# Kernel optimization log

Measured on AMD Instinct MI355X. Metric: run time of the kernel, lower is better.

## Reference

```python
import jax, jax.numpy as jnp
import numpy as np

N_HEADS = 32
N_KV = 8
HEAD_DIM = 128
EPS = 1e-5

def _rope(t, fr, fi):
    # t: [b,s,h,hd] -> pairs [b,s,h,hd/2,2]; fr/fi: [s,hd/2]
    tp = t.astype(jnp.float32).reshape(*t.shape[:-1], HEAD_DIM // 2, 2)
    a, b = tp[..., 0], tp[..., 1]
    fr = fr[None, :, None, :]
    fi = fi[None, :, None, :]
    out = jnp.stack([a * fr - b * fi, a * fi + b * fr], axis=-1)
    return out.reshape(t.shape).astype(t.dtype)

def _rmsnorm(t):
    tf = t.astype(jnp.float32)
    return (tf * jax.lax.rsqrt(jnp.mean(tf * tf, axis=-1, keepdims=True) + EPS)).astype(t.dtype)

def setup_inputs() -> dict:
    key = jax.random.key(0)
    ks = jax.random.split(key, 5)
    b, s, dim = 1, 2048, 4096
    x = jax.random.normal(ks[0], (b, s, dim), dtype=jnp.float32) * 0.02
    wq = jax.random.normal(ks[1], (dim, dim), dtype=jnp.float32) * 0.02
    wk = jax.random.normal(ks[2], (N_KV * HEAD_DIM, dim), dtype=jnp.float32) * 0.02
    wv = jax.random.normal(ks[3], (N_KV * HEAD_DIM, dim), dtype=jnp.float32) * 0.02
    wo = jax.random.normal(ks[4], (dim, dim), dtype=jnp.float32) * 0.02
    # RoPE freqs, llama-style theta=10000
    inv = 1.0 / (10000.0 ** (np.arange(0, HEAD_DIM, 2, dtype=np.float32) / HEAD_DIM))
    ang = np.outer(np.arange(s, dtype=np.float32), inv)  # [s, hd/2]
    freqs_cis = jnp.asarray(np.stack([np.cos(ang), np.sin(ang)], axis=-1))  # [s, hd/2, 2]
    # causal additive mask
    mask = jnp.where(jnp.tril(jnp.ones((s, s), dtype=bool)), 0.0, -1e30).astype(jnp.float32)
    return {"x": x, "wq": wq, "wk": wk, "wv": wv, "wo": wo,
            "freqs_cis": freqs_cis, "mask": mask, "start_pos": 0}

def reference(x, wq, wk, wv, wo, freqs_cis, mask, start_pos):
    b, s, dim = x.shape
    n_rep = N_HEADS // N_KV
    xq = jnp.einsum('bsd,ed->bse', x, wq).reshape(b, s, N_HEADS, HEAD_DIM)
    xk = jnp.einsum('bsd,ed->bse', x, wk).reshape(b, s, N_KV, HEAD_DIM)
    xv = jnp.einsum('bsd,ed->bse', x, wv).reshape(b, s, N_KV, HEAD_DIM)
    fr, fi = freqs_cis[..., 0], freqs_cis[..., 1]
    xq = _rope(xq, fr, fi)
    xk = _rope(xk, fr, fi)
    xq = _rmsnorm(xq)
    xk = _rmsnorm(xk)
    # start_pos=0 prefill: KV cache write/read is identity on xk/xv
    q = xq.transpose(0, 2, 1, 3).reshape(b, N_KV, n_rep, s, HEAD_DIM)  # grouped query heads
    k = xk.transpose(0, 2, 1, 3)  # [b, n_kv, s, hd]
    v = xv.transpose(0, 2, 1, 3)
    scores = jnp.einsum('bkrsd,bktd->bkrst', q, k) / np.sqrt(HEAD_DIM)
    scores = scores + mask[None, None, None, :, :]
    probs = jax.nn.softmax(scores, axis=-1)
    o = jnp.einsum('bkrst,bktd->bkrsd', probs, v)
    o = o.reshape(b, N_HEADS, s, HEAD_DIM).transpose(0, 2, 1, 3).reshape(b, s, dim)
    return jnp.einsum('bse,de->bsd', o, wo)
```

## Files before the change

### kernel.cpp

```cpp
#include <hip/hip_runtime.h>
#include <hip/hip_bf16.h>
#include <cstdint>
#include <cstddef>

using u16 = unsigned short;
using u32 = unsigned int;

typedef __attribute__((ext_vector_type(8))) __bf16 bf16x8;
typedef __attribute__((ext_vector_type(4))) float f32x4;
typedef __attribute__((ext_vector_type(2))) float f32x2;
typedef __attribute__((ext_vector_type(4))) u32 u32x4;

typedef const __attribute__((address_space(1))) void* gas_ptr;
typedef __attribute__((address_space(3))) void* las_ptr;

__device__ __forceinline__ void async_cp16(const void* g, void* l) {
  __builtin_amdgcn_global_load_lds((gas_ptr)g, (las_ptr)l, 16, 0, 0);
}

__device__ __forceinline__ float bf2f(u16 u) {
  u32 v = ((u32)u) << 16;
  return __builtin_bit_cast(float, v);
}
__device__ __forceinline__ u16 f2bf(float f) {
  u32 v = __builtin_bit_cast(u32, f);
  u32 r = (v + 0x7fffu + ((v >> 16) & 1u)) >> 16;
  return (u16)r;
}

__device__ __forceinline__ f32x4 mfma16(bf16x8 a, bf16x8 b, f32x4 c) {
  return __builtin_amdgcn_mfma_f32_16x16x32_bf16(a, b, c, 0, 0, 0);
}

__global__ __launch_bounds__(256) void cvt_f32_bf16(const float* __restrict__ in,
                                                    u16* __restrict__ out, int n8) {
  int i = blockIdx.x * blockDim.x + threadIdx.x;
  int stride = gridDim.x * blockDim.x;
  for (; i < n8; i += stride) {
    const float4* p = (const float4*)(in + (size_t)i * 8);
    float4 a = p[0], b = p[1];
    union { u16 us[8]; u32x4 v; } o;
    o.us[0] = f2bf(a.x); o.us[1] = f2bf(a.y); o.us[2] = f2bf(a.z); o.us[3] = f2bf(a.w);
    o.us[4] = f2bf(b.x); o.us[5] = f2bf(b.y); o.us[6] = f2bf(b.z); o.us[7] = f2bf(b.w);
    *(u32x4*)(out + (size_t)i * 8) = o.v;
  }
}

__global__ __launch_bounds__(256) void cvt4(const float* __restrict__ x,
                                            const float* __restrict__ wq,
                                            const float* __restrict__ wk,
                                            const float* __restrict__ wv,
                                            u16* __restrict__ xb,
                                            u16* __restrict__ wqkv) {
  const int B0 = 1048576;
  const int B1 = B0 + 2097152;
  const int B2 = B1 + 524288;
  const int B3 = B2 + 524288;
  int i = blockIdx.x * blockDim.x + threadIdx.x;
  int stride = gridDim.x * blockDim.x;
  for (; i < B3; i += stride) {
    const float* src; u16* dst; int j;
    if (i < B0)      { src = x;  dst = xb;                           j = i; }
    else if (i < B1) { src = wq; dst = wqkv;                         j = i - B0; }
    else if (i < B2) { src = wk; dst = wqkv + (size_t)4096 * 4096;   j = i - B1; }
    else             { src = wv; dst = wqkv + (size_t)5120 * 4096;   j = i - B2; }
    const float4* p = (const float4*)(src + (size_t)j * 8);
    float4 a = p[0], b = p[1];
    union { u16 us[8]; u32x4 v; } o;
    o.us[0] = f2bf(a.x); o.us[1] = f2bf(a.y); o.us[2] = f2bf(a.z); o.us[3] = f2bf(a.w);
    o.us[4] = f2bf(b.x); o.us[5] = f2bf(b.y); o.us[6] = f2bf(b.z); o.us[7] = f2bf(b.w);
    *(u32x4*)(dst + (size_t)j * 8) = o.v;
  }
}

template <bool F32OUT>
__global__ __launch_bounds__(256, 3) void gemm_bt(const u16* __restrict__ A,
                                                  const u16* __restrict__ B,
                                                  void* __restrict__ Cv,
                                                  int M, int N, int K) {
  __shared__ __align__(16) u16 As[128 * 64];
  __shared__ __align__(16) u16 Bs[128 * 64];
  const int tid = threadIdx.x;
  const int wave = tid >> 6, lane = tid & 63;
  const int quad = lane >> 4, c16 = lane & 15;

  const int mb = M >> 7, nb = N >> 7;
  const int per_xcd_n = nb >> 3;
  const int xcd = blockIdx.x & 7, lid = blockIdx.x >> 3;
  const int m_t = lid % mb, n_local = lid / mb;
  const int m0 = m_t * 128, n0 = (xcd * per_xcd_n + n_local) * 128;

  const int wm = (wave & 1) * 64, wn = (wave >> 1) * 64;

  f32x4 acc[4][4] = {};

  const u16* Ab = A + (size_t)m0 * K;
  const u16* Bb = B + (size_t)n0 * K;

  for (int k0 = 0; k0 < K; k0 += 64) {
    __syncthreads();
#pragma unroll
    for (int i = 0; i < 4; ++i) {
      int idx = tid + 256 * i;
      int row = idx >> 3, sg = (idx & 7) ^ (row & 7);
      async_cp16(Ab + (size_t)row * K + k0 + sg * 8, As + (size_t)idx * 8);
    }
#pragma unroll
    for (int i = 0; i < 4; ++i) {
      int idx = tid + 256 * i;
      int row = idx >> 3, sg = (idx & 7) ^ (row & 7);
      async_cp16(Bb + (size_t)row * K + k0 + sg * 8, Bs + (size_t)idx * 8);
    }
    asm volatile("s_waitcnt vmcnt(0)" ::: "memory");
    __syncthreads();

    bf16x8 af[4][2], bfr[4][2];
#pragma unroll
    for (int mt = 0; mt < 4; ++mt) {
      int row = wm + mt * 16 + c16;
#pragma unroll
      for (int c = 0; c < 2; ++c)
        af[mt][c] = *(const bf16x8*)(As + row * 64 + (((c * 4 + quad) ^ (row & 7)) * 8));
    }
#pragma unroll
    for (int nt = 0; nt < 4; ++nt) {
      int row = wn + nt * 16 + c16;
#pragma unroll
      for (int c = 0; c < 2; ++c)
        bfr[nt][c] = *(const bf16x8*)(Bs + row * 64 + (((c * 4 + quad) ^ (row & 7)) * 8));
    }
#pragma unroll
    for (int c = 0; c < 2; ++c)
#pragma unroll
      for (int mt = 0; mt < 4; ++mt)
#pragma unroll
        for (int nt = 0; nt < 4; ++nt)
          acc[mt][nt] = mfma16(af[mt][c], bfr[nt][c], acc[mt][nt]);
  }

#pragma unroll
  for (int mt = 0; mt < 4; ++mt) {
#pragma unroll
    for (int nt = 0; nt < 4; ++nt) {
#pragma unroll
      for (int r = 0; r < 4; ++r) {
        int gm = m0 + wm + mt * 16 + quad * 4 + r;
        int gn = n0 + wn + nt * 16 + c16;
        float v = acc[mt][nt][r];
        if (F32OUT)
          ((float*)Cv)[(size_t)gm * N + gn] = v;
        else
          ((u16*)Cv)[(size_t)gm * N + gn] = f2bf(v);
      }
    }
  }
}

__global__ __launch_bounds__(256) void transpose_v(const u16* __restrict__ in,
                                                   u16* __restrict__ out) {
  __shared__ __align__(16) u16 t[64 * 72];
  const int bs = blockIdx.x * 64;
  const int be = blockIdx.y * 64;
  const int tid = threadIdx.x;
  {
    const int row = tid >> 3, cc = tid & 7;
#pragma unroll
    for (int pp = 0; pp < 2; ++pp) {
      int r = row + 32 * pp;
      u32x4 v = *(const u32x4*)(in + (size_t)(bs + r) * 6144 + 5120 + be + cc * 8);
      *(u32x4*)(&t[r * 72 + ((cc ^ ((r >> 3) & 7)) * 8)]) = v;
    }
  }
  __syncthreads();
  {
    const int c0 = tid >> 3, rc = tid & 7;
#pragma unroll
    for (int pp = 0; pp < 2; ++pp) {
      int c = c0 + 32 * pp;
      union { u16 us[8]; u32x4 v; } o;
#pragma unroll
      for (int j = 0; j < 8; ++j)
        o.us[j] = t[(rc * 8 + j) * 72 + ((((c >> 3) ^ rc) * 8) + (c & 7))];
      *(u32x4*)(out + (size_t)(be + c) * 2048 + bs + rc * 8) = o.v;
    }
  }
}

__global__ __launch_bounds__(256) void rope_rms(const u16* __restrict__ in, int stride,
                                                u16* __restrict__ out,
                                                const float* __restrict__ freqs,
                                                int n_heads) {
  int gw = blockIdx.x * 4 + (threadIdx.x >> 6);
  int lane = threadIdx.x & 63;
  int s = gw / n_heads, h = gw % n_heads;
  u32 ab = *(const u32*)(in + (size_t)s * stride + h * 128 + lane * 2);
  float a = bf2f((u16)(ab & 0xffff));
  float b = bf2f((u16)(ab >> 16));
  f32x2 ff = *(const f32x2*)(freqs + (size_t)s * 128 + lane * 2);
  float ra = a * ff.x - b * ff.y;
  float rb = a * ff.y + b * ff.x;
  float ss = ra * ra + rb * rb;
#pragma unroll
  for (int m = 32; m; m >>= 1) ss += __shfl_xor(ss, m, 64);
  float r = rsqrtf(ss * (1.0f / 128.0f) + 1e-5f);
  u32 pk = (u32)f2bf(ra * r) | ((u32)f2bf(rb * r) << 16);
  *(u32*)(out + ((size_t)h * 2048 + s) * 128 + lane * 2) = pk;
}

#define SEQ 2048
__global__ __launch_bounds__(512, 2) void attn(const u16* __restrict__ Q,
                                               const u16* __restrict__ Kh,
                                               const u16* __restrict__ VT,
                                               u16* __restrict__ O) {
  __shared__ __align__(16) u16 Ks[2][64 * 128];
  __shared__ __align__(16) u16 Vs[2][128 * 64];
  __shared__ __align__(16) u16 Ps[8][32 * 64];
  const int tid = threadIdx.x;
  const int wave = tid >> 6, lane = tid & 63;
  const int quad = lane >> 4, c16 = lane & 15;
  const int bid = blockIdx.x;
  const int hk = bid & 7;
  const int rest = bid >> 3;
  const int hq = rest & 3;
  const int p = rest >> 2;
  const int h = hk * 4 + hq;

  const int wl = wave & 3, grp = wave >> 2;
  const int qt = grp ? p : (15 - p);
  const int q0w = qt * 128 + wl * 32;
  const int kend = (15 - p) * 128 + 128;

  const float sc = 0.12751743f;
  const float B = 16.5f;
  const u16* Kb = Kh + (size_t)hk * SEQ * 128;
  const u16* Vb = VT + (size_t)hk * 128 * SEQ;

  auto stage = [&](int t0, int b) __attribute__((always_inline)) {
#pragma unroll
    for (int i = 0; i < 2; ++i) {
      int idx = tid + 512 * i;
      int row = idx >> 4, sg = (idx & 15) ^ (row & 7);
      async_cp16(Kb + (size_t)(t0 + row) * 128 + sg * 8, &Ks[b][(size_t)idx * 8]);
    }
#pragma unroll
    for (int i = 0; i < 2; ++i) {
      int idx = tid + 512 * i;
      int row = idx >> 3, sg = (idx & 7) ^ (row & 7);
      async_cp16(Vb + (size_t)row * SEQ + t0 + sg * 8, &Vs[b][(size_t)idx * 8]);
    }
  };

  bf16x8 qfr[2][4];
  const u16* qbase = Q + (size_t)h * SEQ * 128;
#pragma unroll
  for (int g = 0; g < 2; ++g)
#pragma unroll
    for (int c = 0; c < 4; ++c)
      qfr[g][c] =
          *(const bf16x8*)(qbase + (size_t)(q0w + g * 16 + c16) * 128 + c * 32 + quad * 8);

  f32x4 o_acc[2][8] = {};
  float lsum[2][4] = {};

  stage(0, 0);

#pragma unroll 1
  for (int t0 = 0; t0 < kend; t0 += 64) {
    const int cur = (t0 >> 6) & 1;
    asm volatile("s_waitcnt vmcnt(0)" ::: "memory");
    __syncthreads();
    if (t0 + 64 < kend) stage(t0 + 64, cur ^ 1);

    if (t0 < q0w + 32) {
      f32x4 sa[2][4] = {};
      __builtin_amdgcn_s_setprio(1);
#pragma unroll
      for (int ct = 0; ct < 4; ++ct) {
        int t = ct * 16 + c16;
        int tbase = t * 128;
        int tsw = t & 7;
#pragma unroll
        for (int c = 0; c < 4; ++c) {
          bf16x8 kf = *(const bf16x8*)(&Ks[cur][tbase + (((c * 4 + quad) ^ tsw) * 8)]);
          sa[0][ct] = mfma16(qfr[0][c], kf, sa[0][ct]);
          sa[1][ct] = mfma16(qfr[1][c], kf, sa[1][ct]);
        }
      }
      __builtin_amdgcn_s_setprio(0);

      const bool diag = (t0 + 64 > q0w);
      auto soft = [&](bool masked) __attribute__((always_inline)) {
#pragma unroll
        for (int g = 0; g < 2; ++g) {
#pragma unroll
          for (int r = 0; r < 4; ++r) {
            int row = g * 16 + quad * 4 + r;
            int row_q = q0w + row;
            int rbase = row * 64;
            int rsw = row & 7;
#pragma unroll
            for (int ct = 0; ct < 4; ++ct) {
              float s = sa[g][ct][r];
              float arg = fmaf(s, sc, -B);
              if (masked) {
                int t_idx = t0 + ct * 16 + c16;
                arg = (t_idx <= row_q) ? arg : -1.0e30f;
              }
              float pe = exp2f(arg);
              lsum[g][r] += pe;
              u32 pb = (__builtin_bit_cast(u32, pe) + 0x8000u) >> 16;
              Ps[wave][rbase + (((ct * 2 + (c16 >> 3)) ^ rsw) * 8) + (c16 & 7)] = (u16)pb;
            }
          }
        }
      };
      if (diag) soft(true); else soft(false);
      asm volatile("s_waitcnt lgkmcnt(0)" ::: "memory");

      __builtin_amdgcn_s_setprio(1);
#pragma unroll
      for (int tc = 0; tc < 2; ++tc) {
        bf16x8 pf[2];
#pragma unroll
        for (int g = 0; g < 2; ++g) {
          int prow = g * 16 + c16;
          pf[g] = *(const bf16x8*)(&Ps[wave][prow * 64 + (((tc * 4 + quad) ^ (prow & 7)) * 8)]);
        }
#pragma unroll
        for (int nt = 0; nt < 8; ++nt) {
          int dl = nt * 16 + c16;
          bf16x8 vf = *(const bf16x8*)(&Vs[cur][dl * 64 + (((tc * 4 + quad) ^ (dl & 7)) * 8)]);
          o_acc[0][nt] = mfma16(pf[0], vf, o_acc[0][nt]);
          o_acc[1][nt] = mfma16(pf[1], vf, o_acc[1][nt]);
        }
      }
      __builtin_amdgcn_s_setprio(0);
    }
  }

#pragma unroll
  for (int g = 0; g < 2; ++g) {
#pragma unroll
    for (int r = 0; r < 4; ++r) {
      float l = lsum[g][r];
#pragma unroll
      for (int m = 1; m < 16; m <<= 1) l += __shfl_xor(l, m, 64);
      float inv = 1.0f / l;
      int s_idx = q0w + g * 16 + quad * 4 + r;
      u16* ob = O + (size_t)s_idx * 4096 + (size_t)h * 128;
#pragma unroll
      for (int nt = 0; nt < 8; ++nt) ob[nt * 16 + c16] = f2bf(o_acc[g][nt][r] * inv);
    }
  }
}

extern "C" void kernel_launch(void* const* d_in, const int* in_sizes, int n_in,
                              void* d_out, int out_size, void* d_ws, size_t ws_size,
                              hipStream_t stream) {
  const float* x  = (const float*)d_in[0];
  const float* wq = (const float*)d_in[1];
  const float* wk = (const float*)d_in[2];
  const float* wv = (const float*)d_in[3];
  const float* wo = (const float*)d_in[4];
  const float* fr = (const float*)d_in[5];
  float* out = (float*)d_out;

  const size_t S = 2048, D = 4096, KV = 1024, NQKV = D + 2 * KV;
  u16* p = (u16*)d_ws;
  u16* xb     = p; p += S * D;
  u16* wqkv   = p; p += NQKV * D;
  u16* qkvraw = p; p += S * NQKV;
  u16* qh     = p; p += S * D;
  u16* khh    = p; p += S * KV;
  u16* vt     = p; p += KV * S;
  u16* wob = wqkv;
  u16* ob  = qkvraw;

  cvt4<<<dim3(2048), dim3(256), 0, stream>>>(x, wq, wk, wv, xb, wqkv);

  gemm_bt<false><<<dim3((S / 128) * (NQKV / 128)), dim3(256), 0, stream>>>(
      xb, wqkv, (void*)qkvraw, (int)S, (int)NQKV, (int)D);

  {
    int n8 = (int)(D * D / 8);
    cvt_f32_bf16<<<dim3(2048), dim3(256), 0, stream>>>(wo, wob, n8);
  }

  transpose_v<<<dim3(32, 16), dim3(256), 0, stream>>>(qkvraw, vt);
  rope_rms<<<dim3((int)(S * 32 / 4)), dim3(256), 0, stream>>>(qkvraw, (int)NQKV, qh, fr, 32);
  rope_rms<<<dim3((int)(S * 8 / 4)), dim3(256), 0, stream>>>(qkvraw + D, (int)NQKV, khh, fr, 8);

  attn<<<dim3(256), dim3(512), 0, stream>>>(qh, khh, vt, ob);

  gemm_bt<true><<<dim3((S / 128) * (D / 128)), dim3(256), 0, stream>>>(
      ob, wob, (void*)out, (int)S, (int)D, (int)D);
}
```

Baseline: 487.6 us.

## Fuse RoPE, RMSNorm and V transpose into QKV GEMM epilogue

```diff
diff --git a/kernel.cpp b/kernel.cpp
--- a/kernel.cpp
+++ b/kernel.cpp
@@ -5,6 +5,7 @@
 
 using u16 = unsigned short;
 using u32 = unsigned int;
+using u64 = unsigned long long;
 
 typedef __attribute__((ext_vector_type(8))) __bf16 bf16x8;
 typedef __attribute__((ext_vector_type(4))) float f32x4;
@@ -73,11 +74,15 @@
   }
 }
 
-template <bool F32OUT>
+template <int MODE>
 __global__ __launch_bounds__(256, 3) void gemm_bt(const u16* __restrict__ A,
                                                   const u16* __restrict__ B,
                                                   void* __restrict__ Cv,
-                                                  int M, int N, int K) {
+                                                  int M, int N, int K,
+                                                  u16* __restrict__ qh,
+                                                  u16* __restrict__ khh,
+                                                  u16* __restrict__ vt,
+                                                  const float* __restrict__ freqs) {
   __shared__ __align__(16) u16 As[128 * 64];
   __shared__ __align__(16) u16 Bs[128 * 64];
   const int tid = threadIdx.x;
@@ -138,73 +143,87 @@
           acc[mt][nt] = mfma16(af[mt][c], bfr[nt][c], acc[mt][nt]);
   }
 
-#pragma unroll
-  for (int mt = 0; mt < 4; ++mt) {
-#pragma unroll
-    for (int nt = 0; nt < 4; ++nt) {
-#pragma unroll
-      for (int r = 0; r < 4; ++r) {
-        int gm = m0 + wm + mt * 16 + quad * 4 + r;
-        int gn = n0 + wn + nt * 16 + c16;
-        float v = acc[mt][nt][r];
-        if (F32OUT)
-          ((float*)Cv)[(size_t)gm * N + gn] = v;
-        else
-          ((u16*)Cv)[(size_t)gm * N + gn] = f2bf(v);
-      }
-    }
-  }
-}
-
-__global__ __launch_bounds__(256) void transpose_v(const u16* __restrict__ in,
-                                                   u16* __restrict__ out) {
-  __shared__ __align__(16) u16 t[64 * 72];
-  const int bs = blockIdx.x * 64;
-  const int be = blockIdx.y * 64;
-  const int tid = threadIdx.x;
-  {
-    const int row = tid >> 3, cc = tid & 7;
-#pragma unroll
-    for (int pp = 0; pp < 2; ++pp) {
-      int r = row + 32 * pp;
-      u32x4 v = *(const u32x4*)(in + (size_t)(bs + r) * 6144 + 5120 + be + cc * 8);
-      *(u32x4*)(&t[r * 72 + ((cc ^ ((r >> 3) & 7)) * 8)]) = v;
-    }
-  }
-  __syncthreads();
-  {
-    const int c0 = tid >> 3, rc = tid & 7;
-#pragma unroll
-    for (int pp = 0; pp < 2; ++pp) {
-      int c = c0 + 32 * pp;
-      union { u16 us[8]; u32x4 v; } o;
-#pragma unroll
-      for (int j = 0; j < 8; ++j)
-        o.us[j] = t[(rc * 8 + j) * 72 + ((((c >> 3) ^ rc) * 8) + (c & 7))];
-      *(u32x4*)(out + (size_t)(be + c) * 2048 + bs + rc * 8) = o.v;
-    }
-  }
-}
-
-__global__ __launch_bounds__(256) void rope_rms(const u16* __restrict__ in, int stride,
-                                                u16* __restrict__ out,
-                                                const float* __restrict__ freqs,
-                                                int n_heads) {
-  int gw = blockIdx.x * 4 + (threadIdx.x >> 6);
-  int lane = threadIdx.x & 63;
-  int s = gw / n_heads, h = gw % n_heads;
-  u32 ab = *(const u32*)(in + (size_t)s * stride + h * 128 + lane * 2);
-  float a = bf2f((u16)(ab & 0xffff));
-  float b = bf2f((u16)(ab >> 16));
-  f32x2 ff = *(const f32x2*)(freqs + (size_t)s * 128 + lane * 2);
-  float ra = a * ff.x - b * ff.y;
-  float rb = a * ff.y + b * ff.x;
-  float ss = ra * ra + rb * rb;
-#pragma unroll
-  for (int m = 32; m; m >>= 1) ss += __shfl_xor(ss, m, 64);
-  float r = rsqrtf(ss * (1.0f / 128.0f) + 1e-5f);
-  u32 pk = (u32)f2bf(ra * r) | ((u32)f2bf(rb * r) << 16);
-  *(u32*)(out + ((size_t)h * 2048 + s) * 128 + lane * 2) = pk;
+  if constexpr (MODE == 1) {
+#pragma unroll
+    for (int mt = 0; mt < 4; ++mt) {
+#pragma unroll
+      for (int nt = 0; nt < 4; ++nt) {
+#pragma unroll
+        for (int r = 0; r < 4; ++r) {
+          int gm = m0 + wm + mt * 16 + quad * 4 + r;
+          int gn = n0 + wn + nt * 16 + c16;
+          ((float*)Cv)[(size_t)gm * N + gn] = acc[mt][nt][r];
+        }
+      }
+    }
+  } else {
+    __syncthreads();
+    float* sums = (float*)As;
+    if (n0 < 5120) {
+      float ss_arr[4][4];
+#pragma unroll
+      for (int mt = 0; mt < 4; ++mt) {
+#pragma unroll
+        for (int r = 0; r < 4; ++r) {
+          int s = m0 + wm + mt * 16 + quad * 4 + r;
+          const float* fb = freqs + (size_t)s * 128;
+          float ssv = 0.0f;
+#pragma unroll
+          for (int nt = 0; nt < 4; ++nt) {
+            int d = wn + nt * 16 + c16;
+            float v = acc[mt][nt][r];
+            float p = __shfl_xor(v, 1, 64);
+            f32x2 ff = *(const f32x2*)(fb + (d & ~1));
+            float res = (c16 & 1) ? fmaf(v, ff.x, p * ff.y)
+                                  : fmaf(v, ff.x, -p * ff.y);
+            acc[mt][nt][r] = res;
+            ssv = fmaf(res, res, ssv);
+          }
+#pragma unroll
+          for (int m = 1; m < 16; m <<= 1) ssv += __shfl_xor(ssv, m, 64);
+          ss_arr[mt][r] = ssv;
+        }
+      }
+      const int wn_idx = wave >> 1;
+      if (c16 == 0) {
+#pragma unroll
+        for (int mt = 0; mt < 4; ++mt)
+#pragma unroll
+          for (int r = 0; r < 4; ++r)
+            sums[wn_idx * 128 + wm + mt * 16 + quad * 4 + r] = ss_arr[mt][r];
+      }
+      __syncthreads();
+      u16* outb = (n0 < 4096)
+                      ? (qh + (size_t)(n0 >> 7) * M * 128)
+                      : (khh + (size_t)((n0 - 4096) >> 7) * M * 128);
+#pragma unroll
+      for (int mt = 0; mt < 4; ++mt) {
+#pragma unroll
+        for (int r = 0; r < 4; ++r) {
+          int rl = wm + mt * 16 + quad * 4 + r;
+          float tot = ss_arr[mt][r] + sums[(wn_idx ^ 1) * 128 + rl];
+          float scl = rsqrtf(tot * (1.0f / 128.0f) + 1e-5f);
+          int s = m0 + rl;
+#pragma unroll
+          for (int nt = 0; nt < 4; ++nt)
+            outb[(size_t)s * 128 + wn + nt * 16 + c16] = f2bf(acc[mt][nt][r] * scl);
+        }
+      }
+    } else {
+#pragma unroll
+      for (int mt = 0; mt < 4; ++mt) {
+#pragma unroll
+        for (int nt = 0; nt < 4; ++nt) {
+          int dv = (n0 - 5120) + wn + nt * 16 + c16;
+          int s0 = m0 + wm + mt * 16 + quad * 4;
+          union { u16 us[4]; u64 v; } pk;
+#pragma unroll
+          for (int r = 0; r < 4; ++r) pk.us[r] = f2bf(acc[mt][nt][r]);
+          *(u64*)(vt + (size_t)dv * M + s0) = pk.v;
+        }
+      }
+    }
+  }
 }
 
 #define SEQ 2048
@@ -367,31 +386,24 @@
 
   const size_t S = 2048, D = 4096, KV = 1024, NQKV = D + 2 * KV;
   u16* p = (u16*)d_ws;
-  u16* xb     = p; p += S * D;
-  u16* wqkv   = p; p += NQKV * D;
-  u16* qkvraw = p; p += S * NQKV;
-  u16* qh     = p; p += S * D;
-  u16* khh    = p; p += S * KV;
-  u16* vt     = p; p += KV * S;
+  u16* xb   = p; p += S * D;
+  u16* wqkv = p; p += NQKV * D;
+  u16* qh   = p; p += S * D;
+  u16* khh  = p; p += S * KV;
+  u16* vt   = p; p += KV * S;
+  u16* ob   = p; p += S * D;
   u16* wob = wqkv;
-  u16* ob  = qkvraw;
 
   cvt4<<<dim3(2048), dim3(256), 0, stream>>>(x, wq, wk, wv, xb, wqkv);
 
-  gemm_bt<false><<<dim3((S / 128) * (NQKV / 128)), dim3(256), 0, stream>>>(
-      xb, wqkv, (void*)qkvraw, (int)S, (int)NQKV, (int)D);
-
-  {
-    int n8 = (int)(D * D / 8);
-    cvt_f32_bf16<<<dim3(2048), dim3(256), 0, stream>>>(wo, wob, n8);
-  }
-
-  transpose_v<<<dim3(32, 16), dim3(256), 0, stream>>>(qkvraw, vt);
-  rope_rms<<<dim3((int)(S * 32 / 4)), dim3(256), 0, stream>>>(qkvraw, (int)NQKV, qh, fr, 32);
-  rope_rms<<<dim3((int)(S * 8 / 4)), dim3(256), 0, stream>>>(qkvraw + D, (int)NQKV, khh, fr, 8);
+  gemm_bt<2><<<dim3((S / 128) * (NQKV / 128)), dim3(256), 0, stream>>>(
+      xb, wqkv, nullptr, (int)S, (int)NQKV, (int)D, qh, khh, vt, fr);
+
+  cvt_f32_bf16<<<dim3(2048), dim3(256), 0, stream>>>(wo, wob, (int)(D * D / 8));
 
   attn<<<dim3(256), dim3(512), 0, stream>>>(qh, khh, vt, ob);
 
-  gemm_bt<true><<<dim3((S / 128) * (D / 128)), dim3(256), 0, stream>>>(
-      ob, wob, (void*)out, (int)S, (int)D, (int)D);
-}
+  gemm_bt<1><<<dim3((S / 128) * (D / 128)), dim3(256), 0, stream>>>(
+      ob, wob, (void*)out, (int)S, (int)D, (int)D,
+      nullptr, nullptr, nullptr, nullptr);
+}
```

Result: faster. 459.6 us (-5.7%).
